# Kernel tuning notes

Hardware: AMD Instinct MI355X
Metric: run time of the kernel (lower is better)

Reference implementation:

```python
import jax, jax.numpy as jnp
import numpy as np

N, E, F, H, C = 100000, 1600000, 128, 128, 64

def setup_inputs() -> dict:
    key = jax.random.key(0)
    ks = jax.random.split(key, 16)
    def u(k, shape, fan_out):
        s = 1.0 / np.sqrt(fan_out)
        return jax.random.uniform(k, shape, jnp.float32, -s, s)
    return {
        'x': jax.random.normal(ks[0], (N, F), jnp.float32),
        'edge_index': jax.random.randint(ks[1], (2, E), 0, N, jnp.int32),
        # layer 1: F -> H  (stdv = 1/sqrt(out_features); att vecs stdv=1; att_vec stdv=1/sqrt(3))
        'W_low1': u(ks[2], (F, H), H), 'W_high1': u(ks[3], (F, H), H), 'W_mlp1': u(ks[4], (F, H), H),
        'v_low1': u(ks[5], (H, 1), 1), 'v_high1': u(ks[6], (H, 1), 1), 'v_mlp1': u(ks[7], (H, 1), 1),
        'att1': u(ks[8], (3, 3), 3),
        # layer 2: H -> C
        'W_low2': u(ks[9], (H, C), C), 'W_high2': u(ks[10], (H, C), C), 'W_mlp2': u(ks[11], (H, C), C),
        'v_low2': u(ks[12], (C, 1), 1), 'v_high2': u(ks[13], (C, 1), 1), 'v_mlp2': u(ks[14], (C, 1), 1),
        'att2': u(ks[15], (3, 3), 3),
    }

def reference(x, edge_index, W_low1, W_high1, W_mlp1, v_low1, v_high1, v_mlp1, att1,
              W_low2, W_high2, W_mlp2, v_low2, v_high2, v_mlp2, att2):
    row, col = edge_index[0], edge_index[1]
    # row-normalized adjacency: adj_low[i,j] = 1/deg(i); deg==0 rows -> zero output
    deg = jax.ops.segment_sum(jnp.ones((E,), x.dtype), row, num_segments=N)
    inv_deg = jnp.where(deg > 0, 1.0 / jnp.maximum(deg, 1.0), 0.0)[:, None]  # [N,1]

    def spmm_low(h):  # adj_low @ h
        return inv_deg * jax.ops.segment_sum(h[col], row, num_segments=N)

    T = 3.0
    def acm_layer(h, Wl, Wh, Wm, vl, vh, vm, av):
        hl = h @ Wl
        hh = h @ Wh
        out_low = jax.nn.relu(spmm_low(hl))
        out_high = jax.nn.relu(hh - spmm_low(hh))  # adj_high = I - adj_low
        out_mlp = jax.nn.relu(h @ Wm)
        logits = jnp.concatenate([out_low @ vl, out_high @ vh, out_mlp @ vm], axis=1)  # [N,3]
        att = jax.nn.softmax((jax.nn.sigmoid(logits) @ av) / T, axis=1)  # [N,3]
        return 3.0 * (att[:, 0:1] * out_low + att[:, 1:2] * out_high + att[:, 2:3] * out_mlp)

    fea = acm_layer(x, W_low1, W_high1, W_mlp1, v_low1, v_high1, v_mlp1, att1)
    fea = jax.nn.relu(fea)  # dropout is identity at eval
    return acm_layer(fea, W_low2, W_high2, W_mlp2, v_low2, v_high2, v_mlp2, att2)
```

## Files before the change

kernel.cpp:

```cpp
#include <hip/hip_runtime.h>

typedef unsigned short u16;
typedef unsigned int u32;
typedef unsigned long long u64;
typedef __attribute__((ext_vector_type(8))) short short8;
typedef __attribute__((ext_vector_type(4))) float f32x4;
typedef __attribute__((ext_vector_type(4))) u32 u32x4;

#define BSHIFT 8
#define MAXBUCK 512
#define BCAP 8192

__device__ __forceinline__ float bf2f(u32 u) {
    union { u32 i; float f; } v; v.i = u << 16; return v.f;
}
__device__ __forceinline__ float bf2fh(u32 u) {
    union { u32 i; float f; } v; v.i = u & 0xffff0000u; return v.f;
}
__device__ __forceinline__ u16 f2bf(float f) {
    union { float f; u32 i; } v; v.f = f;
    u32 u = (v.i + 0x7fffu + ((v.i >> 16) & 1u)) >> 16;
    return (u16)u;
}

__device__ __forceinline__ int xcd_swz(int bid, int nbg) {
    int q = nbg >> 3, r = nbg & 7;
    int x = bid & 7, i = bid >> 3;
    return (x < r) ? (x * (q + 1) + i) : (r * (q + 1) + (x - r) * q + i);
}

#define CASTBLK 2048
__global__ void k_prep(const float4* __restrict__ X, u32* __restrict__ Xb, long total4,
                       const float* __restrict__ Wl1, const float* __restrict__ Wh1,
                       const float* __restrict__ Wm1, const float* __restrict__ Wl2,
                       const float* __restrict__ Wh2, const float* __restrict__ Wm2,
                       u16* __restrict__ Wp1, u16* __restrict__ Wp2) {
    if (blockIdx.x < CASTBLK) {
        long i = (long)blockIdx.x * blockDim.x + threadIdx.x;
        long stride = (long)CASTBLK * blockDim.x;
        for (; i < total4; i += stride) {
            float4 p = X[i];
            Xb[i * 2 + 0] = (u32)f2bf(p.x) | ((u32)f2bf(p.y) << 16);
            Xb[i * 2 + 1] = (u32)f2bf(p.z) | ((u32)f2bf(p.w) << 16);
        }
        return;
    }
    int tid = (blockIdx.x - CASTBLK) * blockDim.x + threadIdx.x;
    int nthr = 16 * blockDim.x;
    for (int m = 0; m < 8; ++m) {
        int layer = m >> 2;
        int slot = m & 3;
        int Hout = layer ? 64 : 128;
        const float* W = layer ? (slot == 0 ? Wl2 : (slot == 3 ? Wm2 : Wh2))
                               : (slot == 0 ? Wl1 : (slot == 3 ? Wm1 : Wh1));
        float sgn = (slot == 1) ? -1.f : 1.f;
        u16* dst = (layer ? Wp2 : Wp1) + slot * Hout * 128;
        int total = 128 * Hout;
        for (int i = tid; i < total; i += nthr) {
            int T = i / 2048;
            int c = (i / 512) & 3;
            int lane = (i / 8) & 63;
            int j = i & 7;
            int col = T * 16 + (lane & 15);
            int k = c * 32 + (lane >> 4) * 8 + j;
            dst[i] = f2bf(sgn * W[k * Hout + col]);
        }
    }
}

__global__ void k_bscatter_f(const int* __restrict__ erow, const int* __restrict__ ecol, int e,
                             int nbuck, int* __restrict__ gcursor, u32* __restrict__ bedge) {
    __shared__ int hist[MAXBUCK];
    __shared__ int base[MAXBUCK];
    for (int t = threadIdx.x; t < nbuck; t += blockDim.x) hist[t] = 0;
    __syncthreads();
    int chunk = (e + gridDim.x - 1) / gridDim.x;
    int lo = blockIdx.x * chunk, hi = min(e, lo + chunk);
    for (int i = lo + threadIdx.x; i < hi; i += blockDim.x)
        atomicAdd(&hist[erow[i] >> BSHIFT], 1);
    __syncthreads();
    for (int t = threadIdx.x; t < nbuck; t += blockDim.x) {
        int c = hist[t];
        base[t] = c ? atomicAdd(&gcursor[t], c) : 0;
        hist[t] = 0;
    }
    __syncthreads();
    for (int i = lo + threadIdx.x; i < hi; i += blockDim.x) {
        int r = erow[i];
        int bk = r >> BSHIFT;
        int pos = base[bk] + atomicAdd(&hist[bk], 1);
        if (pos < BCAP)
            bedge[(size_t)bk * BCAP + pos] = ((u32)ecol[i] << 8) | (u32)(r & 255);
    }
}

__global__ void k_bscan2(const int* __restrict__ bcnt, int nbuck, int* __restrict__ boff) {
    __shared__ int lds[MAXBUCK];
    int t = threadIdx.x;
    int v = (t < nbuck) ? bcnt[t] : 0;
    lds[t] = v; __syncthreads();
    for (int off = 1; off < MAXBUCK; off <<= 1) {
        int x = (t >= off) ? lds[t - off] : 0;
        __syncthreads();
        lds[t] += x;
        __syncthreads();
    }
    if (t < nbuck) {
        boff[t] = lds[t] - v;
        if (t == nbuck - 1) boff[nbuck] = lds[t];
    }
}

__global__ void k_bfill2f(const u32* __restrict__ bedge, const int* __restrict__ bcnt,
                          const int* __restrict__ boff, int n,
                          int* __restrict__ row_ptr, float* __restrict__ inv_deg,
                          int* __restrict__ cols) {
    __shared__ int cnt[256];
    __shared__ int incl[256];
    __shared__ int pos[256];
    int b = blockIdx.x, t = threadIdx.x;
    cnt[t] = 0;
    __syncthreads();
    int rbase = b << BSHIFT;
    const u32* src = bedge + (size_t)b * BCAP;
    int cb = bcnt[b];
    int lo = boff[b];
    for (int i = t; i < cb; i += 256)
        atomicAdd(&cnt[src[i] & 255u], 1);
    __syncthreads();
    int v = cnt[t];
    incl[t] = v;
    __syncthreads();
    for (int off = 1; off < 256; off <<= 1) {
        int x = (t >= off) ? incl[t - off] : 0;
        __syncthreads();
        incl[t] += x;
        __syncthreads();
    }
    int excl = incl[t] - v;
    pos[t] = excl;
    int row = rbase + t;
    if (row < n) {
        row_ptr[row] = lo + excl;
        inv_deg[row] = v > 0 ? 1.f / (float)v : 0.f;
    }
    if (b == (int)gridDim.x - 1 && t == 0) row_ptr[n] = lo + cb;
    __syncthreads();
    for (int i = t; i < cb; i += 256) {
        u32 vv = src[i];
        int rl = (int)(vv & 255u);
        int p = lo + atomicAdd(&pos[rl], 1);
        cols[p] = (int)(vv >> 8);
    }
}

template<int HOUT, bool L1>
__global__ __launch_bounds__(512)
void k_fused(const u32* __restrict__ X2, const int* __restrict__ row_ptr,
             const int* __restrict__ cols, const float* __restrict__ inv_deg,
             const u16* __restrict__ Wp,
             const float* __restrict__ vl, const float* __restrict__ vh, const float* __restrict__ vm,
             const float* __restrict__ att, int n,
             u16* __restrict__ feaOut, float* __restrict__ fOut) {
    constexpr int WN = HOUT / 16;
    constexpr int WM = 8 / WN;
    constexpr int MT = 4 / WM;
    constexpr int ROWS = 64;
    __shared__ __align__(16) u32 AsU[4096];
    __shared__ __align__(16) u32 AxU[4096];
    int w = threadIdx.x >> 6, lane = threadIdx.x & 63;
    int ql = lane & 15, qi = lane >> 4;
    int wn = w % WN, wm = w / WN;
    int ln15 = lane & 15, lq = lane >> 4;
    int tile = xcd_swz(blockIdx.x, gridDim.x);
    int m0 = tile * ROWS;
    const u32x4* X16 = (const u32x4*)X2;

    for (int rit = 0; rit < 2; ++rit) {
        int rl = w * 8 + rit * 4 + qi;
        int row = m0 + rl;
        int beg = 0, end = 0;
        float s = 0.f;
        u32x4 px = {0u, 0u, 0u, 0u};
        if (row < n) {
            beg = row_ptr[row];
            end = row_ptr[row + 1];
            s = inv_deg[row];
            px = X16[(size_t)row * 16 + ql];
        }
        float a0 = 0.f, a1 = 0.f, a2 = 0.f, a3 = 0.f, a4 = 0.f, a5 = 0.f, a6 = 0.f, a7 = 0.f;
        int myc = (beg + ql < end) ? cols[beg + ql] : 0;
        for (int j0 = beg; j0 < end; j0 += 16) {
            int cnt = end - j0; if (cnt > 16) cnt = 16;
            int nmy = (j0 + 16 + ql < end) ? cols[j0 + 16 + ql] : 0;
            int j = 0;
            for (; j + 8 <= cnt; j += 8) {
                int c0 = __shfl(myc, j + 0, 16);
                int c1 = __shfl(myc, j + 1, 16);
                int c2 = __shfl(myc, j + 2, 16);
                int c3 = __shfl(myc, j + 3, 16);
                int c4 = __shfl(myc, j + 4, 16);
                int c5 = __shfl(myc, j + 5, 16);
                int c6 = __shfl(myc, j + 6, 16);
                int c7 = __shfl(myc, j + 7, 16);
                u32x4 p0 = X16[(size_t)c0 * 16 + ql];
                u32x4 p1 = X16[(size_t)c1 * 16 + ql];
                u32x4 p2 = X16[(size_t)c2 * 16 + ql];
                u32x4 p3 = X16[(size_t)c3 * 16 + ql];
                u32x4 p4 = X16[(size_t)c4 * 16 + ql];
                u32x4 p5 = X16[(size_t)c5 * 16 + ql];
                u32x4 p6 = X16[(size_t)c6 * 16 + ql];
                u32x4 p7 = X16[(size_t)c7 * 16 + ql];
                a0 += bf2f(p0[0] & 0xffffu) + bf2f(p1[0] & 0xffffu) + bf2f(p2[0] & 0xffffu) + bf2f(p3[0] & 0xffffu)
                    + bf2f(p4[0] & 0xffffu) + bf2f(p5[0] & 0xffffu) + bf2f(p6[0] & 0xffffu) + bf2f(p7[0] & 0xffffu);
                a1 += bf2fh(p0[0]) + bf2fh(p1[0]) + bf2fh(p2[0]) + bf2fh(p3[0])
                    + bf2fh(p4[0]) + bf2fh(p5[0]) + bf2fh(p6[0]) + bf2fh(p7[0]);
                a2 += bf2f(p0[1] & 0xffffu) + bf2f(p1[1] & 0xffffu) + bf2f(p2[1] & 0xffffu) + bf2f(p3[1] & 0xffffu)
                    + bf2f(p4[1] & 0xffffu) + bf2f(p5[1] & 0xffffu) + bf2f(p6[1] & 0xffffu) + bf2f(p7[1] & 0xffffu);
                a3 += bf2fh(p0[1]) + bf2fh(p1[1]) + bf2fh(p2[1]) + bf2fh(p3[1])
                    + bf2fh(p4[1]) + bf2fh(p5[1]) + bf2fh(p6[1]) + bf2fh(p7[1]);
                a4 += bf2f(p0[2] & 0xffffu) + bf2f(p1[2] & 0xffffu) + bf2f(p2[2] & 0xffffu) + bf2f(p3[2] & 0xffffu)
                    + bf2f(p4[2] & 0xffffu) + bf2f(p5[2] & 0xffffu) + bf2f(p6[2] & 0xffffu) + bf2f(p7[2] & 0xffffu);
                a5 += bf2fh(p0[2]) + bf2fh(p1[2]) + bf2fh(p2[2]) + bf2fh(p3[2])
                    + bf2fh(p4[2]) + bf2fh(p5[2]) + bf2fh(p6[2]) + bf2fh(p7[2]);
                a6 += bf2f(p0[3] & 0xffffu) + bf2f(p1[3] & 0xffffu) + bf2f(p2[3] & 0xffffu) + bf2f(p3[3] & 0xffffu)
                    + bf2f(p4[3] & 0xffffu) + bf2f(p5[3] & 0xffffu) + bf2f(p6[3] & 0xffffu) + bf2f(p7[3] & 0xffffu);
                a7 += bf2fh(p0[3]) + bf2fh(p1[3]) + bf2fh(p2[3]) + bf2fh(p3[3])
                    + bf2fh(p4[3]) + bf2fh(p5[3]) + bf2fh(p6[3]) + bf2fh(p7[3]);
            }
            for (; j + 4 <= cnt; j += 4) {
                int c0 = __shfl(myc, j + 0, 16);
                int c1 = __shfl(myc, j + 1, 16);
                int c2 = __shfl(myc, j + 2, 16);
                int c3 = __shfl(myc, j + 3, 16);
                u32x4 p0 = X16[(size_t)c0 * 16 + ql];
                u32x4 p1 = X16[(size_t)c1 * 16 + ql];
                u32x4 p2 = X16[(size_t)c2 * 16 + ql];
                u32x4 p3 = X16[(size_t)c3 * 16 + ql];
                a0 += bf2f(p0[0] & 0xffffu) + bf2f(p1[0] & 0xffffu) + bf2f(p2[0] & 0xffffu) + bf2f(p3[0] & 0xffffu);
                a1 += bf2fh(p0[0]) + bf2fh(p1[0]) + bf2fh(p2[0]) + bf2fh(p3[0]);
                a2 += bf2f(p0[1] & 0xffffu) + bf2f(p1[1] & 0xffffu) + bf2f(p2[1] & 0xffffu) + bf2f(p3[1] & 0xffffu);
                a3 += bf2fh(p0[1]) + bf2fh(p1[1]) + bf2fh(p2[1]) + bf2fh(p3[1]);
                a4 += bf2f(p0[2] & 0xffffu) + bf2f(p1[2] & 0xffffu) + bf2f(p2[2] & 0xffffu) + bf2f(p3[2] & 0xffffu);
                a5 += bf2fh(p0[2]) + bf2fh(p1[2]) + bf2fh(p2[2]) + bf2fh(p3[2]);
                a6 += bf2f(p0[3] & 0xffffu) + bf2f(p1[3] & 0xffffu) + bf2f(p2[3] & 0xffffu) + bf2f(p3[3] & 0xffffu);
                a7 += bf2fh(p0[3]) + bf2fh(p1[3]) + bf2fh(p2[3]) + bf2fh(p3[3]);
            }
            for (; j < cnt; ++j) {
                int c = __shfl(myc, j, 16);
                u32x4 p = X16[(size_t)c * 16 + ql];
                a0 += bf2f(p[0] & 0xffffu);
                a1 += bf2fh(p[0]);
                a2 += bf2f(p[1] & 0xffffu);
                a3 += bf2fh(p[1]);
                a4 += bf2f(p[2] & 0xffffu);
                a5 += bf2fh(p[2]);
                a6 += bf2f(p[3] & 0xffffu);
                a7 += bf2fh(p[3]);
            }
            myc = nmy;
        }
        int dl = (rl >> 4) * 1024 + (ql >> 2) * 256 + (ql & 3) * 64 + (rl & 15) * 4;
        u32x4 sv;
        sv[0] = (u32)f2bf(a0 * s) | ((u32)f2bf(a1 * s) << 16);
        sv[1] = (u32)f2bf(a2 * s) | ((u32)f2bf(a3 * s) << 16);
        sv[2] = (u32)f2bf(a4 * s) | ((u32)f2bf(a5 * s) << 16);
        sv[3] = (u32)f2bf(a6 * s) | ((u32)f2bf(a7 * s) << 16);
        *(u32x4*)(AsU + dl) = sv;
        *(u32x4*)(AxU + dl) = px;
    }

    f32x4 acc[MT][3];
#pragma unroll
    for (int mt = 0; mt < MT; ++mt)
#pragma unroll
        for (int g = 0; g < 3; ++g) { f32x4 z = {0.f, 0.f, 0.f, 0.f}; acc[mt][g] = z; }

    __syncthreads();

    const u16* As = (const u16*)AsU;
    const u16* Ax = (const u16*)AxU;
#pragma unroll
    for (int c = 0; c < 4; ++c) {
        size_t fo = (size_t)(wn * 4 + c) * 512 + lane * 8;
        short8 bl  = *(const short8*)(Wp + (size_t)0 * (HOUT * 128) + fo);
        short8 bhn = *(const short8*)(Wp + (size_t)1 * (HOUT * 128) + fo);
        short8 bhp = *(const short8*)(Wp + (size_t)2 * (HOUT * 128) + fo);
        short8 bm  = *(const short8*)(Wp + (size_t)3 * (HOUT * 128) + fo);
#pragma unroll
        for (int mt = 0; mt < MT; ++mt) {
            int rt = wm * MT + mt;
            int lo = (rt * 4 + c) * 512 + lane * 8;
            short8 as = *(const short8*)(As + lo);
            short8 ax = *(const short8*)(Ax + lo);
            acc[mt][0] = __builtin_amdgcn_mfma_f32_16x16x32_bf16(as, bl,  acc[mt][0], 0, 0, 0);
            acc[mt][1] = __builtin_amdgcn_mfma_f32_16x16x32_bf16(as, bhn, acc[mt][1], 0, 0, 0);
            acc[mt][1] = __builtin_amdgcn_mfma_f32_16x16x32_bf16(ax, bhp, acc[mt][1], 0, 0, 0);
            acc[mt][2] = __builtin_amdgcn_mfma_f32_16x16x32_bf16(ax, bm,  acc[mt][2], 0, 0, 0);
        }
    }

    int vcol = wn * 16 + ln15;
    float vv0 = vl[vcol], vv1 = vh[vcol], vv2 = vm[vcol];

    __shared__ float part[WN][3][ROWS];
    __shared__ float wgt[ROWS][3];
#pragma unroll
    for (int mt = 0; mt < MT; ++mt) {
        float pdg[3][4];
#pragma unroll
        for (int g = 0; g < 3; ++g)
#pragma unroll
            for (int r = 0; r < 4; ++r) pdg[g][r] = 0.f;
#pragma unroll
        for (int r = 0; r < 4; ++r) {
            pdg[0][r] += fmaxf(acc[mt][0][r], 0.f) * vv0;
            pdg[1][r] += fmaxf(acc[mt][1][r], 0.f) * vv1;
            pdg[2][r] += fmaxf(acc[mt][2][r], 0.f) * vv2;
        }
#pragma unroll
        for (int off = 1; off < 16; off <<= 1)
#pragma unroll
            for (int g = 0; g < 3; ++g)
#pragma unroll
                for (int r = 0; r < 4; ++r)
                    pdg[g][r] += __shfl_xor(pdg[g][r], off);
        if (ln15 == 0) {
            int rbase = (wm * MT + mt) * 16 + lq * 4;
#pragma unroll
            for (int g = 0; g < 3; ++g)
#pragma unroll
                for (int r = 0; r < 4; ++r)
                    part[wn][g][rbase + r] = pdg[g][r];
        }
    }
    __syncthreads();
    if (threadIdx.x < ROWS) {
        int row = threadIdx.x;
        float d0 = 0.f, d1 = 0.f, d2 = 0.f;
#pragma unroll
        for (int q = 0; q < WN; ++q) {
            d0 += part[q][0][row];
            d1 += part[q][1][row];
            d2 += part[q][2][row];
        }
        float s0 = 1.f / (1.f + __expf(-d0));
        float s1 = 1.f / (1.f + __expf(-d1));
        float s2 = 1.f / (1.f + __expf(-d2));
        float a0 = (s0 * att[0] + s1 * att[3] + s2 * att[6]) * (1.f / 3.f);
        float a1 = (s0 * att[1] + s1 * att[4] + s2 * att[7]) * (1.f / 3.f);
        float a2 = (s0 * att[2] + s1 * att[5] + s2 * att[8]) * (1.f / 3.f);
        float mx = fmaxf(a0, fmaxf(a1, a2));
        float e0 = __expf(a0 - mx), e1 = __expf(a1 - mx), e2 = __expf(a2 - mx);
        float inv = 3.f / (e0 + e1 + e2);
        wgt[row][0] = e0 * inv;
        wgt[row][1] = e1 * inv;
        wgt[row][2] = e2 * inv;
    }
    __syncthreads();

#pragma unroll
    for (int mt = 0; mt < MT; ++mt)
#pragma unroll
        for (int r = 0; r < 4; ++r) {
            int row_local = (wm * MT + mt) * 16 + lq * 4 + r;
            int row = m0 + row_local;
            if (row < n) {
                int col = wn * 16 + ln15;
                float w0 = wgt[row_local][0], w1 = wgt[row_local][1], w2 = wgt[row_local][2];
                float ol = fmaxf(acc[mt][0][r], 0.f);
                float oh = fmaxf(acc[mt][1][r], 0.f);
                float om = fmaxf(acc[mt][2][r], 0.f);
                float val = w0 * ol + w1 * oh + w2 * om;
                if (L1)
                    feaOut[(size_t)row * HOUT + col] = f2bf(fmaxf(val, 0.f));
                else
                    fOut[(size_t)row * HOUT + col] = val;
            }
        }
}

extern "C" void kernel_launch(void* const* d_in, const int* in_sizes, int n_in,
                              void* d_out, int out_size, void* d_ws, size_t ws_size,
                              hipStream_t stream) {
    const int F = 128;
    int n = in_sizes[0] / F;
    int e = in_sizes[1] / 2;
    int n64 = (n + 63) & ~63;
    int nbuck = (n + (1 << BSHIFT) - 1) >> BSHIFT;
    const float* x = (const float*)d_in[0];
    const int* ei = (const int*)d_in[1];
    const int* erow = ei;
    const int* ecol = ei + e;
    const float *Wl1 = (const float*)d_in[2], *Wh1 = (const float*)d_in[3], *Wm1 = (const float*)d_in[4];
    const float *vl1 = (const float*)d_in[5], *vh1 = (const float*)d_in[6], *vm1 = (const float*)d_in[7];
    const float* att1 = (const float*)d_in[8];
    const float *Wl2 = (const float*)d_in[9], *Wh2 = (const float*)d_in[10], *Wm2 = (const float*)d_in[11];
    const float *vl2 = (const float*)d_in[12], *vh2 = (const float*)d_in[13], *vm2 = (const float*)d_in[14];
    const float* att2 = (const float*)d_in[15];
    float* out = (float*)d_out;

    char* ws = (char*)d_ws;
    size_t off = 0;
    auto alloc = [&](size_t b) -> void* {
        void* p = ws + off;
        off = (off + b + 255) & ~(size_t)255;
        return p;
    };
    int* row_ptr = (int*)alloc((size_t)(n + 1) * 4);
    float* inv_deg = (float*)alloc((size_t)n * 4);
    int* gcursor = (int*)alloc(MAXBUCK * 4);
    int* boff = (int*)alloc((MAXBUCK + 1) * 4);
    u32* bedge = (u32*)alloc((size_t)MAXBUCK * BCAP * 4);
    int* cols = (int*)alloc((size_t)e * 4);
    u16* Xb = (u16*)alloc((size_t)n * 128 * 2);
    u16* fea = (u16*)alloc((size_t)n * 128 * 2);
    u16* Wp1 = (u16*)alloc((size_t)4 * 128 * 128 * 2);
    u16* Wp2 = (u16*)alloc((size_t)4 * 64 * 128 * 2);
    (void)ws_size; (void)n_in; (void)out_size; (void)n64;

    k_prep<<<CASTBLK + 16, 256, 0, stream>>>((const float4*)x, (u32*)Xb, (long)n * 32,
                                             Wl1, Wh1, Wm1, Wl2, Wh2, Wm2, Wp1, Wp2);

    hipMemsetAsync(gcursor, 0, (size_t)MAXBUCK * 4, stream);
    k_bscatter_f<<<256, 256, 0, stream>>>(erow, ecol, e, nbuck, gcursor, bedge);
    k_bscan2<<<1, MAXBUCK, 0, stream>>>(gcursor, nbuck, boff);
    k_bfill2f<<<nbuck, 256, 0, stream>>>(bedge, gcursor, boff, n, row_ptr, inv_deg, cols);

    int gb = (n + 63) / 64;

    k_fused<128, true><<<gb, 512, 0, stream>>>((const u32*)Xb, row_ptr, cols, inv_deg,
                                               Wp1, vl1, vh1, vm1, att1, n, fea, nullptr);
    k_fused<64, false><<<gb, 512, 0, stream>>>((const u32*)fea, row_ptr, cols, inv_deg,
                                               Wp2, vl2, vh2, vm2, att2, n, nullptr, out);
}
```

Baseline: 371.6 us.

## Use 32-row tiles with dynamic per-row work claiming and swizzled LDS layout

Shrinks the fused layer kernel to 256-thread blocks handling 32 rows. Quarter-wave groups now claim rows dynamically through an LDS atomic counter instead of a fixed assignment, which should balance the uneven per-row gather cost across waves. The LDS staging layout gains an XOR swizzle to cut bank conflicts on both the stores and the MFMA operand loads. Each wave now covers all rows and a strided set of output columns, which means more accumulators per wave and a smaller block, with occupancy guided by launch bounds.

```diff
diff --git a/kernel.cpp b/kernel.cpp
--- a/kernel.cpp
+++ b/kernel.cpp
@@ -22,6 +22,8 @@
     u32 u = (v.i + 0x7fffu + ((v.i >> 16) & 1u)) >> 16;
     return (u16)u;
 }
+
+__device__ __forceinline__ int swz(int ci) { return ci ^ ((ci >> 4) & 7); }
 
 __device__ __forceinline__ int xcd_swz(int bid, int nbg) {
     int q = nbg >> 3, r = nbg & 7;
@@ -155,30 +157,36 @@
 }
 
 template<int HOUT, bool L1>
-__global__ __launch_bounds__(512)
+__global__ __launch_bounds__(256, 4)
 void k_fused(const u32* __restrict__ X2, const int* __restrict__ row_ptr,
              const int* __restrict__ cols, const float* __restrict__ inv_deg,
              const u16* __restrict__ Wp,
              const float* __restrict__ vl, const float* __restrict__ vh, const float* __restrict__ vm,
              const float* __restrict__ att, int n,
              u16* __restrict__ feaOut, float* __restrict__ fOut) {
-    constexpr int WN = HOUT / 16;
-    constexpr int WM = 8 / WN;
-    constexpr int MT = 4 / WM;
-    constexpr int ROWS = 64;
-    __shared__ __align__(16) u32 AsU[4096];
-    __shared__ __align__(16) u32 AxU[4096];
+    constexpr int KPG = HOUT / 64;
+    constexpr int NTw = 3 * KPG;
+    constexpr int MT = 2;
+    constexpr int ROWS = 32;
+    __shared__ __align__(16) u32 AsU[2048];
+    __shared__ __align__(16) u32 AxU[2048];
+    __shared__ int rctr;
     int w = threadIdx.x >> 6, lane = threadIdx.x & 63;
-    int ql = lane & 15, qi = lane >> 4;
-    int wn = w % WN, wm = w / WN;
+    int ql = lane & 15;
     int ln15 = lane & 15, lq = lane >> 4;
     int tile = xcd_swz(blockIdx.x, gridDim.x);
     int m0 = tile * ROWS;
     const u32x4* X16 = (const u32x4*)X2;
 
-    for (int rit = 0; rit < 2; ++rit) {
-        int rl = w * 8 + rit * 4 + qi;
-        int row = m0 + rl;
+    if (threadIdx.x == 0) rctr = 0;
+    __syncthreads();
+
+    for (;;) {
+        int rv;
+        if (ql == 0) rv = atomicAdd(&rctr, 1);
+        rv = __shfl(rv, 0, 16);
+        if (rv >= ROWS) break;
+        int row = m0 + rv;
         int beg = 0, end = 0;
         float s = 0.f;
         u32x4 px = {0u, 0u, 0u, 0u};
@@ -260,21 +268,23 @@
             }
             myc = nmy;
         }
-        int dl = (rl >> 4) * 1024 + (ql >> 2) * 256 + (ql & 3) * 64 + (rl & 15) * 4;
+        int rr = rv & 15, rt = rv >> 4;
+        int ci = rt * 256 + (ql >> 2) * 64 + (ql & 3) * 16 + rr;
+        int d = swz(ci) * 4;
         u32x4 sv;
         sv[0] = (u32)f2bf(a0 * s) | ((u32)f2bf(a1 * s) << 16);
         sv[1] = (u32)f2bf(a2 * s) | ((u32)f2bf(a3 * s) << 16);
         sv[2] = (u32)f2bf(a4 * s) | ((u32)f2bf(a5 * s) << 16);
         sv[3] = (u32)f2bf(a6 * s) | ((u32)f2bf(a7 * s) << 16);
-        *(u32x4*)(AsU + dl) = sv;
-        *(u32x4*)(AxU + dl) = px;
-    }
-
-    f32x4 acc[MT][3];
+        *(u32x4*)(AsU + d) = sv;
+        *(u32x4*)(AxU + d) = px;
+    }
+
+    f32x4 acc[MT][NTw];
 #pragma unroll
     for (int mt = 0; mt < MT; ++mt)
 #pragma unroll
-        for (int g = 0; g < 3; ++g) { f32x4 z = {0.f, 0.f, 0.f, 0.f}; acc[mt][g] = z; }
+        for (int k = 0; k < NTw; ++k) { f32x4 z = {0.f, 0.f, 0.f, 0.f}; acc[mt][k] = z; }
 
     __syncthreads();
 
@@ -282,28 +292,37 @@
     const u16* Ax = (const u16*)AxU;
 #pragma unroll
     for (int c = 0; c < 4; ++c) {
-        size_t fo = (size_t)(wn * 4 + c) * 512 + lane * 8;
-        short8 bl  = *(const short8*)(Wp + (size_t)0 * (HOUT * 128) + fo);
-        short8 bhn = *(const short8*)(Wp + (size_t)1 * (HOUT * 128) + fo);
-        short8 bhp = *(const short8*)(Wp + (size_t)2 * (HOUT * 128) + fo);
-        short8 bm  = *(const short8*)(Wp + (size_t)3 * (HOUT * 128) + fo);
-#pragma unroll
-        for (int mt = 0; mt < MT; ++mt) {
-            int rt = wm * MT + mt;
-            int lo = (rt * 4 + c) * 512 + lane * 8;
-            short8 as = *(const short8*)(As + lo);
-            short8 ax = *(const short8*)(Ax + lo);
-            acc[mt][0] = __builtin_amdgcn_mfma_f32_16x16x32_bf16(as, bl,  acc[mt][0], 0, 0, 0);
-            acc[mt][1] = __builtin_amdgcn_mfma_f32_16x16x32_bf16(as, bhn, acc[mt][1], 0, 0, 0);
-            acc[mt][1] = __builtin_amdgcn_mfma_f32_16x16x32_bf16(ax, bhp, acc[mt][1], 0, 0, 0);
-            acc[mt][2] = __builtin_amdgcn_mfma_f32_16x16x32_bf16(ax, bm,  acc[mt][2], 0, 0, 0);
-        }
-    }
-
-    int vcol = wn * 16 + ln15;
-    float vv0 = vl[vcol], vv1 = vh[vcol], vv2 = vm[vcol];
-
-    __shared__ float part[WN][3][ROWS];
+#pragma unroll
+        for (int kk = 0; kk < KPG; ++kk) {
+            int T = w + kk * 4;
+            size_t fo = (size_t)(T * 4 + c) * 512 + lane * 8;
+            short8 bl  = *(const short8*)(Wp + (size_t)0 * (HOUT * 128) + fo);
+            short8 bhn = *(const short8*)(Wp + (size_t)1 * (HOUT * 128) + fo);
+            short8 bhp = *(const short8*)(Wp + (size_t)2 * (HOUT * 128) + fo);
+            short8 bm  = *(const short8*)(Wp + (size_t)3 * (HOUT * 128) + fo);
+#pragma unroll
+            for (int mt = 0; mt < MT; ++mt) {
+                int ci = (mt * 4 + c) * 64 + lane;
+                int o = swz(ci) * 8;
+                short8 as = *(const short8*)(As + o);
+                short8 ax = *(const short8*)(Ax + o);
+                acc[mt][0 * KPG + kk] = __builtin_amdgcn_mfma_f32_16x16x32_bf16(as, bl,  acc[mt][0 * KPG + kk], 0, 0, 0);
+                acc[mt][1 * KPG + kk] = __builtin_amdgcn_mfma_f32_16x16x32_bf16(as, bhn, acc[mt][1 * KPG + kk], 0, 0, 0);
+                acc[mt][1 * KPG + kk] = __builtin_amdgcn_mfma_f32_16x16x32_bf16(ax, bhp, acc[mt][1 * KPG + kk], 0, 0, 0);
+                acc[mt][2 * KPG + kk] = __builtin_amdgcn_mfma_f32_16x16x32_bf16(ax, bm,  acc[mt][2 * KPG + kk], 0, 0, 0);
+            }
+        }
+    }
+
+    float vval[NTw];
+#pragma unroll
+    for (int k = 0; k < NTw; ++k) {
+        int g = k / KPG, kk = k % KPG;
+        int col = w * 16 + kk * 64 + ln15;
+        vval[k] = (g == 0 ? vl : (g == 1 ? vh : vm))[col];
+    }
+
+    __shared__ float part[4][3][ROWS];
     __shared__ float wgt[ROWS][3];
 #pragma unroll
     for (int mt = 0; mt < MT; ++mt) {
@@ -313,10 +332,11 @@
 #pragma unroll
             for (int r = 0; r < 4; ++r) pdg[g][r] = 0.f;
 #pragma unroll
-        for (int r = 0; r < 4; ++r) {
-            pdg[0][r] += fmaxf(acc[mt][0][r], 0.f) * vv0;
-            pdg[1][r] += fmaxf(acc[mt][1][r], 0.f) * vv1;
-            pdg[2][r] += fmaxf(acc[mt][2][r], 0.f) * vv2;
+        for (int k = 0; k < NTw; ++k) {
+            int g = k / KPG;
+#pragma unroll
+            for (int r = 0; r < 4; ++r)
+                pdg[g][r] += fmaxf(acc[mt][k][r], 0.f) * vval[k];
         }
 #pragma unroll
         for (int off = 1; off < 16; off <<= 1)
@@ -326,12 +346,12 @@
                 for (int r = 0; r < 4; ++r)
                     pdg[g][r] += __shfl_xor(pdg[g][r], off);
         if (ln15 == 0) {
-            int rbase = (wm * MT + mt) * 16 + lq * 4;
+            int rbase = mt * 16 + lq * 4;
 #pragma unroll
             for (int g = 0; g < 3; ++g)
 #pragma unroll
                 for (int r = 0; r < 4; ++r)
-                    part[wn][g][rbase + r] = pdg[g][r];
+                    part[w][g][rbase + r] = pdg[g][r];
         }
     }
     __syncthreads();
@@ -339,7 +359,7 @@
         int row = threadIdx.x;
         float d0 = 0.f, d1 = 0.f, d2 = 0.f;
 #pragma unroll
-        for (int q = 0; q < WN; ++q) {
+        for (int q = 0; q < 4; ++q) {
             d0 += part[q][0][row];
             d1 += part[q][1][row];
             d2 += part[q][2][row];
@@ -362,22 +382,24 @@
 #pragma unroll
     for (int mt = 0; mt < MT; ++mt)
 #pragma unroll
-        for (int r = 0; r < 4; ++r) {
-            int row_local = (wm * MT + mt) * 16 + lq * 4 + r;
-            int row = m0 + row_local;
-            if (row < n) {
-                int col = wn * 16 + ln15;
-                float w0 = wgt[row_local][0], w1 = wgt[row_local][1], w2 = wgt[row_local][2];
-                float ol = fmaxf(acc[mt][0][r], 0.f);
-                float oh = fmaxf(acc[mt][1][r], 0.f);
-                float om = fmaxf(acc[mt][2][r], 0.f);
-                float val = w0 * ol + w1 * oh + w2 * om;
-                if (L1)
-                    feaOut[(size_t)row * HOUT + col] = f2bf(fmaxf(val, 0.f));
-                else
-                    fOut[(size_t)row * HOUT + col] = val;
+        for (int kk = 0; kk < KPG; ++kk)
+#pragma unroll
+            for (int r = 0; r < 4; ++r) {
+                int row_local = mt * 16 + lq * 4 + r;
+                int row = m0 + row_local;
+                if (row < n) {
+                    int col = w * 16 + kk * 64 + ln15;
+                    float w0 = wgt[row_local][0], w1 = wgt[row_local][1], w2 = wgt[row_local][2];
+                    float ol = fmaxf(acc[mt][0 * KPG + kk][r], 0.f);
+                    float oh = fmaxf(acc[mt][1 * KPG + kk][r], 0.f);
+                    float om = fmaxf(acc[mt][2 * KPG + kk][r], 0.f);
+                    float val = w0 * ol + w1 * oh + w2 * om;
+                    if (L1)
+                        feaOut[(size_t)row * HOUT + col] = f2bf(fmaxf(val, 0.f));
+                    else
+                        fOut[(size_t)row * HOUT + col] = val;
+                }
             }
-        }
 }
 
 extern "C" void kernel_launch(void* const* d_in, const int* in_sizes, int n_in,
@@ -386,7 +408,6 @@
     const int F = 128;
     int n = in_sizes[0] / F;
     int e = in_sizes[1] / 2;
-    int n64 = (n + 63) & ~63;
     int nbuck = (n + (1 << BSHIFT) - 1) >> BSHIFT;
     const float* x = (const float*)d_in[0];
     const int* ei = (const int*)d_in[1];
@@ -417,7 +438,7 @@
     u16* fea = (u16*)alloc((size_t)n * 128 * 2);
     u16* Wp1 = (u16*)alloc((size_t)4 * 128 * 128 * 2);
     u16* Wp2 = (u16*)alloc((size_t)4 * 64 * 128 * 2);
-    (void)ws_size; (void)n_in; (void)out_size; (void)n64;
+    (void)ws_size; (void)n_in; (void)out_size;
 
     k_prep<<<CASTBLK + 16, 256, 0, stream>>>((const float4*)x, (u32*)Xb, (long)n * 32,
                                              Wl1, Wh1, Wm1, Wl2, Wh2, Wm2, Wp1, Wp2);
@@ -427,10 +448,10 @@
     k_bscan2<<<1, MAXBUCK, 0, stream>>>(gcursor, nbuck, boff);
     k_bfill2f<<<nbuck, 256, 0, stream>>>(bedge, gcursor, boff, n, row_ptr, inv_deg, cols);
 
-    int gb = (n + 63) / 64;
-
-    k_fused<128, true><<<gb, 512, 0, stream>>>((const u32*)Xb, row_ptr, cols, inv_deg,
+    int gb = (n + 31) / 32;
+
+    k_fused<128, true><<<gb, 256, 0, stream>>>((const u32*)Xb, row_ptr, cols, inv_deg,
                                                Wp1, vl1, vh1, vm1, att1, n, fea, nullptr);
-    k_fused<64, false><<<gb, 512, 0, stream>>>((const u32*)fea, row_ptr, cols, inv_deg,
+    k_fused<64, false><<<gb, 256, 0, stream>>>((const u32*)fea, row_ptr, cols, inv_deg,
                                                Wp2, vl2, vh2, vm2, att2, n, nullptr, out);
 }
```

New measurement: 344.9 us. 1.08x faster.
